# Kernel tuning notes

Hardware: AMD Instinct MI355X
Metric: run time of the kernel (lower is better)

Reference implementation:

```python
import jax, jax.numpy as jnp
import numpy as np
import math

K = 8       # wavelet order (k)
C = 8       # channels (c)
ALPHA = 64  # retained Fourier modes
L = 0       # coarsest level
B = 32
N = 8192    # power of two


def setup_inputs() -> dict:
    key = jax.random.key(0)
    ks = jax.random.split(key, 14)
    ck = C * K
    scale = 1.0 / (ck * ck)  # matches torch: 1/(c*k)**2
    f32 = jnp.float32
    inp = {
        "x": jax.random.normal(ks[0], (B, N, C, K), dtype=f32),
        # SparseKernelFT1d weights (complex, stored as re/im): scale * rand
        "wA_re": scale * jax.random.uniform(ks[1], (ck, ck, ALPHA), dtype=f32),
        "wA_im": scale * jax.random.uniform(ks[2], (ck, ck, ALPHA), dtype=f32),
        "wB_re": scale * jax.random.uniform(ks[3], (ck, ck, ALPHA), dtype=f32),
        "wB_im": scale * jax.random.uniform(ks[4], (ck, ck, ALPHA), dtype=f32),
        "wC_re": scale * jax.random.uniform(ks[5], (ck, ck, ALPHA), dtype=f32),
        "wC_im": scale * jax.random.uniform(ks[6], (ck, ck, ALPHA), dtype=f32),
        # T0 linear layer (k -> k)
        "T0_w": jax.random.normal(ks[7], (K, K), dtype=f32) / math.sqrt(K),
        "T0_b": 0.01 * jax.random.normal(ks[8], (K,), dtype=f32),
        # Legendre wavelet filter buffers: ec_* are [H0.T;H1.T] / [G0.T;G1.T] (2k,k),
        # rc_* are [H0;G0] / [H1;G1] (2k,k). Stand-ins: random orthonormal-ish matrices
        # scaled like wavelet filters (same math regardless of exact values).
        "ec_s": jax.random.normal(ks[9], (2 * K, K), dtype=f32) / math.sqrt(2 * K),
        "ec_d": jax.random.normal(ks[10], (2 * K, K), dtype=f32) / math.sqrt(2 * K),
        "rc_e": jax.random.normal(ks[11], (2 * K, K), dtype=f32) / math.sqrt(2 * K),
        "rc_o": jax.random.normal(ks[12], (2 * K, K), dtype=f32) / math.sqrt(2 * K),
    }
    return inp


def _sparse_ft(x, w_re, w_im):
    # x: [B, N, c, k] -> spectral mixing over first ALPHA rfft modes
    Bb, Nn, c, k = x.shape
    xv = x.reshape(Bb, Nn, c * k).transpose(0, 2, 1)   # [B, ck, N]
    xf = jnp.fft.rfft(xv)                               # [B, ck, N//2+1] complex
    l = min(ALPHA, Nn // 2 + 1)
    W = (w_re[:, :, :l] + 1j * w_im[:, :, :l]).astype(jnp.complex64)
    of = jnp.einsum('bix,iox->box', xf[:, :, :l], W)
    out_ft = jnp.zeros((Bb, c * k, Nn // 2 + 1), dtype=jnp.complex64).at[:, :, :l].set(of)
    xo = jnp.fft.irfft(out_ft, n=Nn)                    # [B, ck, N] real
    return xo.transpose(0, 2, 1).reshape(Bb, Nn, c, k)


def reference(x, wA_re, wA_im, wB_re, wB_im, wC_re, wC_im, T0_w, T0_b,
              ec_s, ec_d, rc_e, rc_o):
    Bb, Nn, c, k = x.shape
    ns = int(math.floor(math.log2(Nn)))
    Ud, Us = [], []
    # --- decomposition ---
    for _ in range(ns - L):
        xa = jnp.concatenate([x[:, ::2], x[:, 1::2]], axis=-1)  # [B, N/2, c, 2k]
        d = xa @ ec_d                                           # [B, N/2, c, k]
        s = xa @ ec_s
        Ud.append(_sparse_ft(d, wA_re, wA_im) + _sparse_ft(s, wB_re, wB_im))
        Us.append(_sparse_ft(d, wC_re, wC_im))
        x = s
    # --- coarsest-level linear ---
    x = x @ T0_w.T + T0_b
    # --- reconstruction (u_s is None branch) ---
    for i in range(ns - 1 - L, -1, -1):
        x = x + Us[i]
        xc = jnp.concatenate([x, Ud[i]], axis=-1)               # [B, n, c, 2k]
        x_e = xc @ rc_e
        x_o = xc @ rc_o
        Bc, Nc, cc, _ = xc.shape
        x = jnp.stack([x_e, x_o], axis=2).reshape(Bc, Nc * 2, cc, K)  # interleave even/odd
    return (x,) + tuple(Ud) + tuple(Us)
```

## Files before the change

### kernel.cpp

```cpp
#include <hip/hip_runtime.h>

#define BB 32
#define CKD 64
#define CC 8
#define KK 8
#define FPW 132

__device__ const int D_FCB[14] = {0,32,48,56,60,62,63,64,65,66,67,68,69,70};
__device__ const int D_TB[14] = {0,64,96,112,120,124,126,127,128,129,130,131,132,133};
__device__ const int D_L[13]  = {64,64,64,64,64,64,33,17,9,5,3,2,1};
__device__ const int D_FTOF[13] = {0,524288,786432,917504,983040,1015808,1032192,
                                   1048576,1064960,1081344,1097728,1114112,1130496};
__device__ const int D_XP[65] = {0,13,25,36,46,56,65,74,83,92,100,108,116,124,132,140,
    148,156,163,170,177,184,191,198,205,212,219,226,233,240,247,254,261,268,274,280,
    286,292,298,304,310,316,322,328,334,340,346,352,358,364,370,376,382,388,394,400,
    406,412,418,424,430,436,442,448,454};

typedef __attribute__((ext_vector_type(4))) short s4v;
typedef __attribute__((ext_vector_type(8))) short s8v;
typedef __attribute__((ext_vector_type(4))) float f4v;

static __device__ __forceinline__ float4 ld4(const float* p){ return *(const float4*)p; }
static __device__ __forceinline__ size_t d_udo(int i){ return 33554432ull - (16777216u >> i); }
static __device__ __forceinline__ size_t d_uso(int i){ return 50329600ull - (16777216u >> i); }
static __device__ __forceinline__ size_t d_tof(int i){ return 128ull * (8192u - (8192u >> i)); }

static __device__ __forceinline__ unsigned short b16(float f) {
    unsigned u = __float_as_uint(f);
    u += 0x7FFFu + ((u >> 16) & 1u);
    return (unsigned short)(u >> 16);
}
static __device__ __forceinline__ float fb16(unsigned short h) {
    return __uint_as_float(((unsigned)h) << 16);
}

__global__ __launch_bounds__(256) void gen_tbl2_k(unsigned short* __restrict__ Th,
        unsigned short* __restrict__ Tl, unsigned short* __restrict__ Tfh,
        unsigned short* __restrict__ Tfl) {
    int lvl = blockIdx.y;
    int nh = 4096 >> lvl;
    int idx = blockIdx.x * 256 + threadIdx.x;
    if (blockIdx.z == 0) {
        if (idx >= nh * 128) return;
        int t = idx >> 7, k = idx & 127, x = k >> 1;
        int l = nh / 2 + 1; if (l > 64) l = 64;
        float v = 0.f;
        if (x < l) {
            int r = (x * t) & (nh - 1);
            float th = 6.283185307179586f * ((float)r / (float)nh);
            float s, c; sincosf(th, &s, &c);
            v = (k & 1) ? s : c;
        }
        unsigned short hi = b16(v);
        unsigned short lo = b16(v - fb16(hi));
        size_t off = d_tof(lvl) + idx;
        Th[off] = hi; Tl[off] = lo;
    } else {
        int nhp = nh < 128 ? 128 : nh;
        if (idx >= 128 * nhp) return;
        int j = idx & 7;
        int lane = (idx >> 3) & 63;
        int mt = (idx >> 9) & 7;
        int kb = idx >> 12;
        int row = mt*16 + (lane & 15);
        int t = kb*32 + (lane >> 4)*8 + j;
        int x = row >> 1;
        int l = nh / 2 + 1; if (l > 64) l = 64;
        float v = 0.f;
        if (x < l && t < nh) {
            int r = (x * t) & (nh - 1);
            float th = 6.283185307179586f * ((float)r / (float)nh);
            float s, c; sincosf(th, &s, &c);
            v = (row & 1) ? -s : c;
        }
        unsigned short hi = b16(v);
        unsigned short lo = b16(v - fb16(hi));
        size_t off = (size_t)D_FTOF[lvl] + idx;
        Tfh[off] = hi; Tfl[off] = lo;
    }
}

__global__ __launch_bounds__(256) void wtr_k(const float* __restrict__ wAr,
        const float* __restrict__ wAi, const float* __restrict__ wBr,
        const float* __restrict__ wBi, const float* __restrict__ wCr,
        const float* __restrict__ wCi, float* __restrict__ wt) {
    int x = blockIdx.x, arr = blockIdx.y;
    const float* W;
    switch (arr) {
        case 0: W = wAr; break;
        case 1: W = wAi; break;
        case 2: W = wBr; break;
        case 3: W = wBi; break;
        case 4: W = wCr; break;
        default: W = wCi; break;
    }
    float* o = wt + ((size_t)arr*64 + x)*4096;
    for (int q = threadIdx.x; q < 4096; q += 256)
        o[q] = W[(size_t)q*64 + x];
}

__global__ __launch_bounds__(256) void decomp_k(const float* __restrict__ xin,
        const float* __restrict__ ecd, const float* __restrict__ ecs,
        float* __restrict__ dslot, float* __restrict__ sslot, int nh) {
    int idx = blockIdx.x * 256 + threadIdx.x;
    if (idx >= BB * nh * CC) return;
    int c = idx & 7;
    int t = (idx >> 3) % nh;
    int b = idx / (nh * CC);
    const float* p0 = xin + ((size_t)b * 2 * nh + 2 * t) * CKD + c * KK;
    float xa[16];
    float4 v;
    v = ld4(p0);      xa[0]=v.x; xa[1]=v.y; xa[2]=v.z; xa[3]=v.w;
    v = ld4(p0+4);    xa[4]=v.x; xa[5]=v.y; xa[6]=v.z; xa[7]=v.w;
    v = ld4(p0+64);   xa[8]=v.x; xa[9]=v.y; xa[10]=v.z; xa[11]=v.w;
    v = ld4(p0+68);   xa[12]=v.x; xa[13]=v.y; xa[14]=v.z; xa[15]=v.w;
    float dd[8], ss[8];
    #pragma unroll
    for (int m = 0; m < 8; m++) { dd[m] = 0.f; ss[m] = 0.f; }
    #pragma unroll
    for (int j = 0; j < 16; j++) {
        float xv = xa[j];
        #pragma unroll
        for (int m = 0; m < 8; m++) {
            dd[m] = fmaf(xv, ecd[j*8+m], dd[m]);
            ss[m] = fmaf(xv, ecs[j*8+m], ss[m]);
        }
    }
    size_t ob = ((size_t)b * nh + t) * CKD + c * KK;
    *(float4*)(dslot+ob)   = make_float4(dd[0],dd[1],dd[2],dd[3]);
    *(float4*)(dslot+ob+4) = make_float4(dd[4],dd[5],dd[6],dd[7]);
    *(float4*)(sslot+ob)   = make_float4(ss[0],ss[1],ss[2],ss[3]);
    *(float4*)(sslot+ob+4) = make_float4(ss[4],ss[5],ss[6],ss[7]);
}

__global__ __launch_bounds__(256) void decomp_small_k(const float* __restrict__ s4base,
        const float* __restrict__ ecd, const float* __restrict__ ecs,
        const float* __restrict__ T0w, const float* __restrict__ T0b,
        float* __restrict__ outbuf, float* __restrict__ xt0) {
    __shared__ float sA[128*64];
    __shared__ float sB[64*64];
    int b = blockIdx.x, tid = threadIdx.x;
    for (int lvl = 5; lvl <= 12; lvl++) {
        int nh = 4096 >> lvl;
        const float* src = (lvl == 5) ? (s4base + (size_t)b*256*CKD)
                                      : (((lvl - 6) & 1) ? sB : sA);
        float* dst = ((lvl - 5) & 1) ? sB : sA;
        float* dG = outbuf + d_udo(lvl) + (size_t)b*nh*CKD;
        float* sG = outbuf + d_uso(lvl) + (size_t)b*nh*CKD;
        for (int q = tid; q < nh*8; q += 256) {
            int c = q & 7, t = q >> 3;
            const float* p0 = src + (size_t)(2*t)*CKD + c*KK;
            float xa[16];
            float4 v;
            v = ld4(p0);      xa[0]=v.x; xa[1]=v.y; xa[2]=v.z; xa[3]=v.w;
            v = ld4(p0+4);    xa[4]=v.x; xa[5]=v.y; xa[6]=v.z; xa[7]=v.w;
            v = ld4(p0+64);   xa[8]=v.x; xa[9]=v.y; xa[10]=v.z; xa[11]=v.w;
            v = ld4(p0+68);   xa[12]=v.x; xa[13]=v.y; xa[14]=v.z; xa[15]=v.w;
            float dd[8], ss[8];
            #pragma unroll
            for (int m = 0; m < 8; m++) { dd[m] = 0.f; ss[m] = 0.f; }
            #pragma unroll
            for (int j = 0; j < 16; j++) {
                float xv = xa[j];
                #pragma unroll
                for (int m = 0; m < 8; m++) {
                    dd[m] = fmaf(xv, ecd[j*8+m], dd[m]);
                    ss[m] = fmaf(xv, ecs[j*8+m], ss[m]);
                }
            }
            size_t ob = (size_t)t * CKD + c * KK;
            *(float4*)(dG+ob)   = make_float4(dd[0],dd[1],dd[2],dd[3]);
            *(float4*)(dG+ob+4) = make_float4(dd[4],dd[5],dd[6],dd[7]);
            *(float4*)(sG+ob)   = make_float4(ss[0],ss[1],ss[2],ss[3]);
            *(float4*)(sG+ob+4) = make_float4(ss[4],ss[5],ss[6],ss[7]);
            float* dl = dst + t*CKD + c*KK;
            #pragma unroll
            for (int j = 0; j < 8; j++) dl[j] = ss[j];
        }
        __syncthreads();
    }
    if (tid < 64) {
        int m = tid & 7, c = tid >> 3;
        const float* xr = sB + c*KK;
        float a = T0b[m];
        #pragma unroll
        for (int j = 0; j < 8; j++) a = fmaf(xr[j], T0w[m*8+j], a);
        xt0[(size_t)b*64 + tid] = a;
    }
}

__global__ __launch_bounds__(256) void fft_fwd_mfma_k(const float* __restrict__ outbuf,
        const unsigned short* __restrict__ Tfh, const unsigned short* __restrict__ Tfl,
        float* __restrict__ xfpf, float2* __restrict__ xf_all) {
    __shared__ unsigned vp[128*FPW];
    int slot = blockIdx.x;
    int lvl = 0;
    while (lvl < 12 && slot >= D_FCB[lvl+1]) lvl++;
    int nh = 4096 >> lvl;
    int ch = D_FCB[lvl+1] - D_FCB[lvl];
    int t0s = (slot - D_FCB[lvl]) * 128;
    int b = blockIdx.y;
    const float* V0 = outbuf + d_udo(lvl) + (size_t)b * nh * CKD;
    const float* V1 = outbuf + d_uso(lvl) + (size_t)b * nh * CKD;
    const unsigned short* THb = Tfh + D_FTOF[lvl];
    const unsigned short* TLb = Tfl + D_FTOF[lvl];
    int tid = threadIdx.x;
    int w = tid >> 6, lane = tid & 63;
    int col = lane & 15, khi = lane >> 4;
    int mt0 = w * 2;
    #pragma unroll
    for (int q = 0; q < 16; q++) {
        int fi = tid + 256*q;
        int tl_ = fi >> 5;
        int t = t0s + tl_;
        int iq = fi & 31;
        int z = iq >> 4;
        int i4 = (iq & 15) * 4;
        const float* Vz = z ? V1 : V0;
        float4 v = make_float4(0.f,0.f,0.f,0.f);
        if (t < nh) v = ld4(Vz + (size_t)t*CKD + i4);
        const float* pv = &v.x;
        int rowb = z*64 + i4;
        #pragma unroll
        for (int j = 0; j < 4; j++) {
            int row = rowb + j;
            float f = pv[j];
            unsigned u = __float_as_uint(f);
            unsigned hi = u & 0xFFFF0000u;
            float r = f - __uint_as_float(hi);
            unsigned lo = __float_as_uint(r) & 0xFFFF0000u;
            int cw = tl_ ^ (((row >> 3) & 7) << 2);
            vp[row*FPW + cw] = (hi >> 16) | lo;
        }
    }
    __syncthreads();
    int rrow[8], rswz[8];
    #pragma unroll
    for (int n = 0; n < 8; n++) {
        rrow[n] = n*16 + col;
        rswz[n] = ((rrow[n] >> 3) & 7) << 2;
    }
    f4v acc[2][8];
    #pragma unroll
    for (int m = 0; m < 2; m++)
        #pragma unroll
        for (int n = 0; n < 8; n++) acc[m][n] = (f4v){0.f,0.f,0.f,0.f};
    int kb0 = (slot - D_FCB[lvl]) * 4;
    #pragma unroll
    for (int kk = 0; kk < 4; kk++) {
        int kb = kb0 + kk;
        s8v ah[2], al[2];
        #pragma unroll
        for (int m = 0; m < 2; m++) {
            size_t fo = (((size_t)kb*8 + (mt0 + m))*64 + lane)*8;
            ah[m] = *(const s8v*)(THb + fo);
            al[m] = *(const s8v*)(TLb + fo);
        }
        int cb = kk*32 + khi*8;
        #pragma unroll
        for (int n = 0; n < 8; n++) {
            const unsigned* pr = vp + rrow[n]*FPW;
            uint4 w0 = *(const uint4*)(pr + (cb ^ rswz[n]));
            uint4 w1 = *(const uint4*)(pr + ((cb + 4) ^ rswz[n]));
            s8v bh, bl;
            const unsigned* pw = &w0.x;
            #pragma unroll
            for (int j = 0; j < 4; j++) {
                bh[j] = (short)(pw[j] & 0xFFFFu);
                bl[j] = (short)(pw[j] >> 16);
            }
            pw = &w1.x;
            #pragma unroll
            for (int j = 0; j < 4; j++) {
                bh[4+j] = (short)(pw[j] & 0xFFFFu);
                bl[4+j] = (short)(pw[j] >> 16);
            }
            #pragma unroll
            for (int m = 0; m < 2; m++) {
                acc[m][n] = __builtin_amdgcn_mfma_f32_16x16x32_bf16(ah[m], bh, acc[m][n], 0,0,0);
                acc[m][n] = __builtin_amdgcn_mfma_f32_16x16x32_bf16(ah[m], bl, acc[m][n], 0,0,0);
                acc[m][n] = __builtin_amdgcn_mfma_f32_16x16x32_bf16(al[m], bh, acc[m][n], 0,0,0);
            }
        }
    }
    if (ch == 1) {
        float* XB = (float*)xf_all + (size_t)lvl*524288 + (size_t)b*16384;
        #pragma unroll
        for (int m = 0; m < 2; m++) {
            int m0 = (mt0 + m)*16 + khi*4;
            #pragma unroll
            for (int n = 0; n < 8; n++) {
                int ic = n*16 + col;
                int z = ic >> 6, i = ic & 63;
                float* X = XB + (size_t)z*8192;
                #pragma unroll
                for (int r = 0; r < 4; r++) {
                    int row = m0 + r;
                    X[(((size_t)(row >> 1)*64 + i) << 1) | (row & 1)] = acc[m][n][r];
                }
            }
        }
    } else {
        #pragma unroll
        for (int m = 0; m < 2; m++) {
            int m0 = (mt0 + m)*16 + khi*4;
            #pragma unroll
            for (int n = 0; n < 8; n++) {
                int ic = n*16 + col;
                int z = ic >> 6, i = ic & 63;
                float* P = xfpf + ((size_t)slot*64 + (size_t)b*2 + z) * 8192;
                #pragma unroll
                for (int r = 0; r < 4; r++)
                    P[(size_t)(m0 + r)*64 + i] = acc[m][n][r];
            }
        }
    }
}

__global__ __launch_bounds__(256) void reduce_fwd_k(const float* __restrict__ xfpf,
        float2* __restrict__ xf_all) {
    int lvl = blockIdx.y;
    int e = blockIdx.x * 256 + threadIdx.x;
    int j = e & 4095;
    int bz = e >> 12;
    int x = j >> 6, i = j & 63;
    int c0 = D_FCB[lvl], c1 = D_FCB[lvl+1];
    float re = 0.f, im = 0.f;
    for (int c = c0; c < c1; c++) {
        size_t base = ((size_t)c*64 + bz) * 8192;
        re += xfpf[base + (size_t)(2*x)*64 + i];
        im += xfpf[base + (size_t)(2*x+1)*64 + i];
    }
    xf_all[(size_t)lvl*262144 + (size_t)bz*4096 + j] = make_float2(re, im);
}

__global__ __launch_bounds__(512) void mix_all_k(const float2* __restrict__ xf_all,
        const float* __restrict__ wt,
        unsigned short* __restrict__ ofh, unsigned short* __restrict__ ofl) {
    int x = 0;
    while (x < 64 && (int)blockIdx.x >= D_XP[x+1]) x++;
    int lvl = blockIdx.x - D_XP[x];
    int nh = 4096 >> lvl;
    const float2* xfL = xf_all + (size_t)lvl*262144;
    int tid = threadIdx.x;
    int o = tid & 63, wq = tid >> 6;
    __shared__ float2 sxd[BB*CKD];
    __shared__ float2 sxs[BB*CKD];
    __shared__ float  swt[6][16*CKD];
    for (int q = tid; q < BB*CKD; q += 512) {
        int b = q >> 6, i = q & 63;
        sxd[q] = xfL[((size_t)b*2 + 0)*4096 + x*64 + i];
        sxs[q] = xfL[((size_t)b*2 + 1)*4096 + x*64 + i];
    }
    float2 aud[4], aus[4];
    #pragma unroll
    for (int j=0;j<4;j++){ aud[j]=make_float2(0.f,0.f); aus[j]=make_float2(0.f,0.f); }
    const float* WTx = wt + (size_t)x*4096;
    for (int ic = 0; ic < 4; ic++) {
        __syncthreads();
        for (int q = tid; q < 6*1024; q += 512) {
            int arr = q >> 10, r = q & 1023;
            swt[arr][r] = WTx[(size_t)arr*262144 + ic*1024 + r];
        }
        __syncthreads();
        #pragma unroll 4
        for (int ii = 0; ii < 16; ii++) {
            float ar = swt[0][ii*64+o], ai_ = swt[1][ii*64+o];
            float br = swt[2][ii*64+o], bi_ = swt[3][ii*64+o];
            float cr = swt[4][ii*64+o], ci_ = swt[5][ii*64+o];
            int i = ic*16 + ii;
            #pragma unroll
            for (int j = 0; j < 4; j++) {
                float2 xd = sxd[(wq*4+j)*64 + i];
                float2 xs = sxs[(wq*4+j)*64 + i];
                aud[j].x += xd.x*ar - xd.y*ai_ + xs.x*br - xs.y*bi_;
                aud[j].y += xd.x*ai_ + xd.y*ar + xs.x*bi_ + xs.y*br;
                aus[j].x += xd.x*cr - xd.y*ci_;
                aus[j].y += xd.x*ci_ + xd.y*cr;
            }
        }
    }
    float w = (x == 0 || 2*x == nh) ? 1.f : 2.f;
    float sc = w / (float)nh;
    int k0 = 2*x;
    #pragma unroll
    for (int j = 0; j < 4; j++) {
        int b = wq*4 + j;
        {
            size_t base = (((size_t)lvl*32 + b)*2 + 0)*8192;
            float A = sc*aud[j].x, Bn = -sc*aud[j].y;
            unsigned short ha = b16(A),  hb = b16(Bn);
            unsigned short la = b16(A - fb16(ha)), lb = b16(Bn - fb16(hb));
            ofh[base + (size_t)k0*64 + o]     = ha;
            ofh[base + (size_t)(k0+1)*64 + o] = hb;
            ofl[base + (size_t)k0*64 + o]     = la;
            ofl[base + (size_t)(k0+1)*64 + o] = lb;
        }
        {
            size_t base = (((size_t)lvl*32 + b)*2 + 1)*8192;
            float A = sc*aus[j].x, Bn = -sc*aus[j].y;
            unsigned short ha = b16(A),  hb = b16(Bn);
            unsigned short la = b16(A - fb16(ha)), lb = b16(Bn - fb16(hb));
            ofh[base + (size_t)k0*64 + o]     = ha;
            ofh[base + (size_t)(k0+1)*64 + o] = hb;
            ofl[base + (size_t)k0*64 + o]     = la;
            ofl[base + (size_t)(k0+1)*64 + o] = lb;
        }
    }
}

__global__ __launch_bounds__(256) void fft_inv_mfma_k(
        const unsigned short* __restrict__ ofh, const unsigned short* __restrict__ ofl,
        const unsigned short* __restrict__ Th,  const unsigned short* __restrict__ Tl,
        float* __restrict__ outbuf) {
    __shared__ unsigned short gh[2*64*132];
    __shared__ unsigned short gl[2*64*132];
    int lvl = 0;
    while (lvl < 12 && (int)blockIdx.x >= D_TB[lvl+1]) lvl++;
    int g = blockIdx.x - D_TB[lvl];
    int nh = 4096 >> lvl;
    int tbase = g * 64;
    int b = blockIdx.y;
    int tid = threadIdx.x;
    #pragma unroll
    for (int q = 0; q < 8; q++) {
        int fi = tid + 256*q;
        int z = fi >> 10;
        int r = fi & 1023;
        int k = r & 127, oct = r >> 7;
        const unsigned short* Gh = ofh + (((size_t)lvl*32 + b)*2 + z)*8192;
        const unsigned short* Gl = ofl + (((size_t)lvl*32 + b)*2 + z)*8192;
        uint4 vh = *(const uint4*)(Gh + (size_t)k*64 + oct*8);
        uint4 vl = *(const uint4*)(Gl + (size_t)k*64 + oct*8);
        const unsigned* ph = &vh.x;
        const unsigned* pl = &vl.x;
        #pragma unroll
        for (int i = 0; i < 8; i++) {
            unsigned wd = ph[i>>1];
            gh[z*8448 + (oct*8+i)*132 + k] = (i&1) ? (unsigned short)(wd>>16) : (unsigned short)(wd&0xFFFF);
            wd = pl[i>>1];
            gl[z*8448 + (oct*8+i)*132 + k] = (i&1) ? (unsigned short)(wd>>16) : (unsigned short)(wd&0xFFFF);
        }
    }
    __syncthreads();
    int w = tid >> 6;
    int lane = tid & 63;
    int tb = tbase + w*16;
    if (tb >= nh) return;
    int trow = lane & 15, khi = lane >> 4;
    int tA = tb + trow; if (tA >= nh) tA = nh - 1;
    const unsigned short* THp = Th + d_tof(lvl) + (size_t)tA*128 + khi*8;
    const unsigned short* TLp = Tl + d_tof(lvl) + (size_t)tA*128 + khi*8;
    f4v acc[8];
    #pragma unroll
    for (int n = 0; n < 8; n++) acc[n] = (f4v){0.f,0.f,0.f,0.f};
    #pragma unroll
    for (int kk = 0; kk < 4; kk++) {
        s8v ah = *(const s8v*)(THp + kk*32);
        s8v al = *(const s8v*)(TLp + kk*32);
        #pragma unroll
        for (int n = 0; n < 8; n++) {
            int z = n >> 2;
            int off = z*8448 + ((n & 3)*16 + trow)*132 + kk*32 + khi*8;
            s4v b0 = *(const s4v*)(gh + off);
            s4v b1 = *(const s4v*)(gh + off + 4);
            s4v c0 = *(const s4v*)(gl + off);
            s4v c1 = *(const s4v*)(gl + off + 4);
            s8v bh = __builtin_shufflevector(b0, b1, 0,1,2,3,4,5,6,7);
            s8v bl = __builtin_shufflevector(c0, c1, 0,1,2,3,4,5,6,7);
            acc[n] = __builtin_amdgcn_mfma_f32_16x16x32_bf16(ah, bh, acc[n], 0, 0, 0);
            acc[n] = __builtin_amdgcn_mfma_f32_16x16x32_bf16(ah, bl, acc[n], 0, 0, 0);
            acc[n] = __builtin_amdgcn_mfma_f32_16x16x32_bf16(al, bh, acc[n], 0, 0, 0);
        }
    }
    float* U0 = outbuf + d_udo(lvl) + (size_t)b * nh * CKD;
    float* U1 = outbuf + d_uso(lvl) + (size_t)b * nh * CKD;
    int thi4 = khi * 4;
    #pragma unroll
    for (int n = 0; n < 8; n++) {
        float* U = (n >> 2) ? U1 : U0;
        int ocol = (n & 3)*16 + trow;
        #pragma unroll
        for (int r = 0; r < 4; r++) {
            int t = tb + thi4 + r;
            if (t < nh) U[(size_t)t*64 + ocol] = acc[n][r];
        }
    }
}

__global__ __launch_bounds__(256) void recon_small_k(const float* __restrict__ xt0,
        const float* __restrict__ outbuf,
        const float* __restrict__ rce, const float* __restrict__ rco,
        float* __restrict__ rb0) {
    __shared__ float xA[128*64];
    __shared__ float xB[64*64];
    int b = blockIdx.x, tid = threadIdx.x;
    if (tid < 64) xB[tid] = xt0[(size_t)b*64 + tid];
    __syncthreads();
    for (int i = 12; i >= 6; i--) {
        int nh = 4096 >> i;
        const float* cur = ((i == 12) || !(i & 1)) ? xB : xA;
        float* nxt = (i & 1) ? xB : xA;
        const float* Us = outbuf + d_uso(i) + (size_t)b*nh*CKD;
        const float* Ud = outbuf + d_udo(i) + (size_t)b*nh*CKD;
        for (int q = tid; q < nh*8; q += 256) {
            int c = q & 7, t = q >> 3;
            size_t base = (size_t)t*CKD + c*KK;
            float xc[16];
            float4 a0 = ld4(cur+base), a1 = ld4(cur+base+4);
            float4 u0 = ld4(Us+base),  u1 = ld4(Us+base+4);
            float4 d0 = ld4(Ud+base),  d1 = ld4(Ud+base+4);
            xc[0]=a0.x+u0.x; xc[1]=a0.y+u0.y; xc[2]=a0.z+u0.z; xc[3]=a0.w+u0.w;
            xc[4]=a1.x+u1.x; xc[5]=a1.y+u1.y; xc[6]=a1.z+u1.z; xc[7]=a1.w+u1.w;
            xc[8]=d0.x;  xc[9]=d0.y;  xc[10]=d0.z; xc[11]=d0.w;
            xc[12]=d1.x; xc[13]=d1.y; xc[14]=d1.z; xc[15]=d1.w;
            float e[8], o2[8];
            #pragma unroll
            for (int m = 0; m < 8; m++) { e[m] = 0.f; o2[m] = 0.f; }
            #pragma unroll
            for (int j = 0; j < 16; j++) {
                float xv = xc[j];
                #pragma unroll
                for (int m = 0; m < 8; m++) {
                    e[m]  = fmaf(xv, rce[j*8+m], e[m]);
                    o2[m] = fmaf(xv, rco[j*8+m], o2[m]);
                }
            }
            if (i > 6) {
                float* pe = nxt + (size_t)(2*t)*CKD + c*KK;
                #pragma unroll
                for (int j = 0; j < 8; j++) { pe[j] = e[j]; pe[CKD + j] = o2[j]; }
            } else {
                float* pe = rb0 + ((size_t)b*128 + 2*t)*CKD + c*KK;
                *(float4*)(pe)      = make_float4(e[0],e[1],e[2],e[3]);
                *(float4*)(pe+4)    = make_float4(e[4],e[5],e[6],e[7]);
                *(float4*)(pe+64)   = make_float4(o2[0],o2[1],o2[2],o2[3]);
                *(float4*)(pe+68)   = make_float4(o2[4],o2[5],o2[6],o2[7]);
            }
        }
        __syncthreads();
    }
}

__global__ __launch_bounds__(256) void recon_k(const float* __restrict__ xin,
        const float* __restrict__ us, const float* __restrict__ ud,
        const float* __restrict__ rce, const float* __restrict__ rco,
        float* __restrict__ xout, int nh) {
    int idx = blockIdx.x*256 + threadIdx.x;
    if (idx >= BB*nh*CC) return;
    int c = idx & 7;
    int t = (idx >> 3) % nh;
    int b = idx / (nh*CC);
    size_t base = ((size_t)b*nh + t)*CKD + c*KK;
    float xc[16];
    float4 a0 = ld4(xin+base), a1 = ld4(xin+base+4);
    float4 u0 = ld4(us+base),  u1 = ld4(us+base+4);
    float4 d0 = ld4(ud+base),  d1 = ld4(ud+base+4);
    xc[0]=a0.x+u0.x; xc[1]=a0.y+u0.y; xc[2]=a0.z+u0.z; xc[3]=a0.w+u0.w;
    xc[4]=a1.x+u1.x; xc[5]=a1.y+u1.y; xc[6]=a1.z+u1.z; xc[7]=a1.w+u1.w;
    xc[8]=d0.x;  xc[9]=d0.y;  xc[10]=d0.z; xc[11]=d0.w;
    xc[12]=d1.x; xc[13]=d1.y; xc[14]=d1.z; xc[15]=d1.w;
    float e[8], o2[8];
    #pragma unroll
    for (int m = 0; m < 8; m++) { e[m] = 0.f; o2[m] = 0.f; }
    #pragma unroll
    for (int j = 0; j < 16; j++) {
        float xv = xc[j];
        #pragma unroll
        for (int m = 0; m < 8; m++) {
            e[m]  = fmaf(xv, rce[j*8+m], e[m]);
            o2[m] = fmaf(xv, rco[j*8+m], o2[m]);
        }
    }
    size_t ob = ((size_t)b*2*nh + 2*t)*CKD + c*KK;
    *(float4*)(xout+ob)      = make_float4(e[0],e[1],e[2],e[3]);
    *(float4*)(xout+ob+4)    = make_float4(e[4],e[5],e[6],e[7]);
    *(float4*)(xout+ob+64)   = make_float4(o2[0],o2[1],o2[2],o2[3]);
    *(float4*)(xout+ob+68)   = make_float4(o2[4],o2[5],o2[6],o2[7]);
}

extern "C" void kernel_launch(void* const* d_in, const int* in_sizes, int n_in,
                              void* d_out, int out_size, void* d_ws, size_t ws_size,
                              hipStream_t stream) {
    const float* x   = (const float*)d_in[0];
    const float* wAr = (const float*)d_in[1];
    const float* wAi = (const float*)d_in[2];
    const float* wBr = (const float*)d_in[3];
    const float* wBi = (const float*)d_in[4];
    const float* wCr = (const float*)d_in[5];
    const float* wCi = (const float*)d_in[6];
    const float* T0w = (const float*)d_in[7];
    const float* T0b = (const float*)d_in[8];
    const float* ecs = (const float*)d_in[9];
    const float* ecd = (const float*)d_in[10];
    const float* rce = (const float*)d_in[11];
    const float* rco = (const float*)d_in[12];
    float* out = (float*)d_out;
    float* wsf = (float*)d_ws;

    size_t p = 0;
    float2* xf_all = (float2*)(wsf + p); p += 6815744;
    unsigned short* ofh = (unsigned short*)(wsf + p); p += 3407872;
    unsigned short* ofl = (unsigned short*)(wsf + p); p += 3407872;
    unsigned short* Th  = (unsigned short*)(wsf + p); p += 528384;
    unsigned short* Tl  = (unsigned short*)(wsf + p); p += 528384;
    unsigned short* Tfh = (unsigned short*)(wsf + p); p += 573440;
    unsigned short* Tfl = (unsigned short*)(wsf + p); p += 573440;
    float*  wt   = wsf + p; p += 1572864;
    float*  xt0  = wsf + p; p += 2048;
    float*  rb0  = wsf + p; p += 4194304;
    float*  rb1  = wsf + p; p += 8388608;
    float*  xfpf = wsf + p; p += 36700160;
    (void)ws_size; (void)in_sizes; (void)n_in; (void)out_size;

    size_t udo[13], uso[13];
    for (int i = 0; i < 13; i++) {
        udo[i] = 33554432ull - (16777216u >> i);
        uso[i] = 50329600ull - (16777216u >> i);
    }

    gen_tbl2_k<<<dim3(2048, 13, 2), 256, 0, stream>>>(Th, Tl, Tfh, Tfl);
    wtr_k<<<dim3(64, 6), 256, 0, stream>>>(wAr, wAi, wBr, wBi, wCr, wCi, wt);

    for (int i = 0; i < 5; i++) {
        int nh = 4096 >> i;
        const float* xin_l = (i == 0) ? x : (out + uso[i-1]);
        int tot = BB * nh * CC;
        decomp_k<<<(tot + 255)/256, 256, 0, stream>>>(xin_l, ecd, ecs, out + udo[i], out + uso[i], nh);
    }
    decomp_small_k<<<BB, 256, 0, stream>>>(out + uso[4], ecd, ecs, T0w, T0b, out, xt0);

    fft_fwd_mfma_k<<<dim3(70, BB), 256, 0, stream>>>(out, Tfh, Tfl, xfpf, xf_all);
    reduce_fwd_k<<<dim3(1024, 5), 256, 0, stream>>>(xfpf, xf_all);
    mix_all_k<<<454, 512, 0, stream>>>(xf_all, wt, ofh, ofl);
    fft_inv_mfma_k<<<dim3(133, BB), 256, 0, stream>>>(ofh, ofl, Th, Tl, out);

    recon_small_k<<<BB, 256, 0, stream>>>(xt0, out, rce, rco, rb0);
    const float* rin = rb0;
    for (int i = 5; i >= 0; i--) {
        int nh = 4096 >> i;
        float* ro = (i == 0) ? out : ((i & 1) ? rb1 : rb0);
        int tot = BB * nh * CC;
        recon_k<<<(tot + 255)/256, 256, 0, stream>>>(rin, out + uso[i], out + udo[i], rce, rco, ro, nh);
        rin = ro;
    }
}
```

Baseline: 477.1 us.

## Run spectral mixing as split-bf16 MFMA GEMM with prepacked real-block weights

Replaces the scalar FP32 complex spectral-mixing kernel with an MFMA kernel. The complex products for the A, B and C weights become one 256x256 real block matrix. That matrix is prepacked per mode into hi/lo bf16 fragments by a new wbig_k kernel. Activations are split into hi/lo bf16 in swizzled shared memory, and three MFMAs per tile approximate FP32 accuracy. This is meant to remove the FP32 FMA bottleneck of the mixing stage, at the cost of an extra packing kernel, about 16 MB more weight traffic, and some zero blocks in the GEMM.

```diff
diff --git a/kernel.cpp b/kernel.cpp
--- a/kernel.cpp
+++ b/kernel.cpp
@@ -97,6 +97,45 @@
     float* o = wt + ((size_t)arr*64 + x)*4096;
     for (int q = threadIdx.x; q < 4096; q += 256)
         o[q] = W[(size_t)q*64 + x];
+}
+
+__global__ __launch_bounds__(256) void wbig_k(const float* __restrict__ wt,
+        unsigned short* __restrict__ wbh, unsigned short* __restrict__ wbl) {
+    int x = blockIdx.x;
+    int f0 = blockIdx.y * 2048;
+    for (int q = threadIdx.x; q < 2048; q += 256) {
+        int f = f0 + q;
+        int j = f & 7;
+        int lane = (f >> 3) & 63;
+        int nt = (f >> 9) & 15;
+        int kt = f >> 13;
+        int k = kt*32 + (lane >> 4)*8 + j;
+        int n = nt*16 + (lane & 15);
+        int pk = k >> 6, i = k & 63;
+        int pn = n >> 6, o = n & 63;
+        int arr; float sgn;
+        switch ((pn << 2) | pk) {
+            case 0:  arr = 0; sgn =  1.f; break;
+            case 1:  arr = 1; sgn = -1.f; break;
+            case 2:  arr = 2; sgn =  1.f; break;
+            case 3:  arr = 3; sgn = -1.f; break;
+            case 4:  arr = 1; sgn = -1.f; break;
+            case 5:  arr = 0; sgn = -1.f; break;
+            case 6:  arr = 3; sgn = -1.f; break;
+            case 7:  arr = 2; sgn = -1.f; break;
+            case 8:  arr = 4; sgn =  1.f; break;
+            case 9:  arr = 5; sgn = -1.f; break;
+            case 12: arr = 5; sgn = -1.f; break;
+            case 13: arr = 4; sgn = -1.f; break;
+            default: arr = -1; sgn = 0.f; break;
+        }
+        float v = 0.f;
+        if (arr >= 0) v = sgn * wt[((size_t)arr*64 + x)*4096 + (size_t)i*64 + o];
+        unsigned short h = b16(v);
+        unsigned short l2 = b16(v - fb16(h));
+        wbh[(size_t)x*65536 + f] = h;
+        wbl[(size_t)x*65536 + f] = l2;
+    }
 }
 
 __global__ __launch_bounds__(256) void decomp_k(const float* __restrict__ xin,
@@ -334,77 +373,92 @@
     xf_all[(size_t)lvl*262144 + (size_t)bz*4096 + j] = make_float2(re, im);
 }
 
-__global__ __launch_bounds__(512) void mix_all_k(const float2* __restrict__ xf_all,
-        const float* __restrict__ wt,
+__global__ __launch_bounds__(256) void mix_mfma_k(const float2* __restrict__ xf_all,
+        const unsigned short* __restrict__ wbh, const unsigned short* __restrict__ wbl,
         unsigned short* __restrict__ ofh, unsigned short* __restrict__ ofl) {
+    __shared__ unsigned ax[32*260];
     int x = 0;
     while (x < 64 && (int)blockIdx.x >= D_XP[x+1]) x++;
     int lvl = blockIdx.x - D_XP[x];
     int nh = 4096 >> lvl;
     const float2* xfL = xf_all + (size_t)lvl*262144;
     int tid = threadIdx.x;
-    int o = tid & 63, wq = tid >> 6;
-    __shared__ float2 sxd[BB*CKD];
-    __shared__ float2 sxs[BB*CKD];
-    __shared__ float  swt[6][16*CKD];
-    for (int q = tid; q < BB*CKD; q += 512) {
-        int b = q >> 6, i = q & 63;
-        sxd[q] = xfL[((size_t)b*2 + 0)*4096 + x*64 + i];
-        sxs[q] = xfL[((size_t)b*2 + 1)*4096 + x*64 + i];
-    }
-    float2 aud[4], aus[4];
-    #pragma unroll
-    for (int j=0;j<4;j++){ aud[j]=make_float2(0.f,0.f); aus[j]=make_float2(0.f,0.f); }
-    const float* WTx = wt + (size_t)x*4096;
-    for (int ic = 0; ic < 4; ic++) {
-        __syncthreads();
-        for (int q = tid; q < 6*1024; q += 512) {
-            int arr = q >> 10, r = q & 1023;
-            swt[arr][r] = WTx[(size_t)arr*262144 + ic*1024 + r];
-        }
-        __syncthreads();
-        #pragma unroll 4
-        for (int ii = 0; ii < 16; ii++) {
-            float ar = swt[0][ii*64+o], ai_ = swt[1][ii*64+o];
-            float br = swt[2][ii*64+o], bi_ = swt[3][ii*64+o];
-            float cr = swt[4][ii*64+o], ci_ = swt[5][ii*64+o];
-            int i = ic*16 + ii;
-            #pragma unroll
-            for (int j = 0; j < 4; j++) {
-                float2 xd = sxd[(wq*4+j)*64 + i];
-                float2 xs = sxs[(wq*4+j)*64 + i];
-                aud[j].x += xd.x*ar - xd.y*ai_ + xs.x*br - xs.y*bi_;
-                aud[j].y += xd.x*ai_ + xd.y*ar + xs.x*bi_ + xs.y*br;
-                aus[j].x += xd.x*cr - xd.y*ci_;
-                aus[j].y += xd.x*ci_ + xd.y*cr;
-            }
-        }
-    }
-    float w = (x == 0 || 2*x == nh) ? 1.f : 2.f;
-    float sc = w / (float)nh;
+    for (int q = tid; q < 4096; q += 256) {
+        int b = q >> 7, z = (q >> 6) & 1, i = q & 63;
+        float2 v = xfL[((size_t)b*2 + z)*4096 + (size_t)x*64 + i];
+        int sw = ((b >> 3) & 7) << 2;
+        int kR = z*128 + i;
+        unsigned uR = __float_as_uint(v.x);
+        unsigned hiR = uR & 0xFFFF0000u;
+        float rR = v.x - __uint_as_float(hiR);
+        unsigned loR = __float_as_uint(rR) & 0xFFFF0000u;
+        ax[b*260 + (kR ^ sw)] = (hiR >> 16) | loR;
+        unsigned uI = __float_as_uint(v.y);
+        unsigned hiI = uI & 0xFFFF0000u;
+        float rI = v.y - __uint_as_float(hiI);
+        unsigned loI = __float_as_uint(rI) & 0xFFFF0000u;
+        ax[b*260 + ((kR + 64) ^ sw)] = (hiI >> 16) | loI;
+    }
+    __syncthreads();
+    int w4 = tid >> 6, lane = tid & 63;
+    int col = lane & 15, khi = lane >> 4;
+    int mt = w4 & 1, nt0 = (w4 >> 1) * 8;
+    int arow = mt*16 + col;
+    int asw = ((arow >> 3) & 7) << 2;
+    const unsigned* ap = ax + arow*260;
+    const unsigned short* WBH = wbh + (size_t)x*65536;
+    const unsigned short* WBL = wbl + (size_t)x*65536;
+    f4v acc[8];
+    #pragma unroll
+    for (int n = 0; n < 8; n++) acc[n] = (f4v){0.f,0.f,0.f,0.f};
+    #pragma unroll
+    for (int kt = 0; kt < 8; kt++) {
+        int cb = kt*32 + khi*8;
+        uint4 a0 = *(const uint4*)(ap + (cb ^ asw));
+        uint4 a1 = *(const uint4*)(ap + ((cb + 4) ^ asw));
+        s8v ah, al;
+        const unsigned* pw = &a0.x;
+        #pragma unroll
+        for (int j = 0; j < 4; j++) {
+            ah[j] = (short)(pw[j] & 0xFFFFu);
+            al[j] = (short)(pw[j] >> 16);
+        }
+        pw = &a1.x;
+        #pragma unroll
+        for (int j = 0; j < 4; j++) {
+            ah[4+j] = (short)(pw[j] & 0xFFFFu);
+            al[4+j] = (short)(pw[j] >> 16);
+        }
+        #pragma unroll
+        for (int n = 0; n < 8; n++) {
+            int nt = nt0 + n;
+            size_t fo = (((size_t)kt*16 + nt)*64 + lane)*8;
+            s8v bh = *(const s8v*)(WBH + fo);
+            s8v bl = *(const s8v*)(WBL + fo);
+            acc[n] = __builtin_amdgcn_mfma_f32_16x16x32_bf16(ah, bh, acc[n], 0, 0, 0);
+            acc[n] = __builtin_amdgcn_mfma_f32_16x16x32_bf16(ah, bl, acc[n], 0, 0, 0);
+            acc[n] = __builtin_amdgcn_mfma_f32_16x16x32_bf16(al, bh, acc[n], 0, 0, 0);
+        }
+    }
+    float wfac = (x == 0 || 2*x == nh) ? 1.f : 2.f;
+    float sc = wfac / (float)nh;
     int k0 = 2*x;
     #pragma unroll
-    for (int j = 0; j < 4; j++) {
-        int b = wq*4 + j;
-        {
-            size_t base = (((size_t)lvl*32 + b)*2 + 0)*8192;
-            float A = sc*aud[j].x, Bn = -sc*aud[j].y;
-            unsigned short ha = b16(A),  hb = b16(Bn);
-            unsigned short la = b16(A - fb16(ha)), lb = b16(Bn - fb16(hb));
-            ofh[base + (size_t)k0*64 + o]     = ha;
-            ofh[base + (size_t)(k0+1)*64 + o] = hb;
-            ofl[base + (size_t)k0*64 + o]     = la;
-            ofl[base + (size_t)(k0+1)*64 + o] = lb;
-        }
-        {
-            size_t base = (((size_t)lvl*32 + b)*2 + 1)*8192;
-            float A = sc*aus[j].x, Bn = -sc*aus[j].y;
-            unsigned short ha = b16(A),  hb = b16(Bn);
-            unsigned short la = b16(A - fb16(ha)), lb = b16(Bn - fb16(hb));
-            ofh[base + (size_t)k0*64 + o]     = ha;
-            ofh[base + (size_t)(k0+1)*64 + o] = hb;
-            ofl[base + (size_t)k0*64 + o]     = la;
-            ofl[base + (size_t)(k0+1)*64 + o] = lb;
+    for (int n = 0; n < 8; n++) {
+        int nn = nt0 + n;
+        int pn = nn >> 2;
+        int o = (nn & 3)*16 + col;
+        int z = pn >> 1;
+        int kr = k0 + (pn & 1);
+        #pragma unroll
+        for (int r = 0; r < 4; r++) {
+            int b = mt*16 + khi*4 + r;
+            size_t base = (((size_t)lvl*32 + b)*2 + z)*8192 + (size_t)kr*64 + o;
+            float v = sc * acc[n][r];
+            unsigned short h = b16(v);
+            unsigned short l2 = b16(v - fb16(h));
+            ofh[base] = h;
+            ofl[base] = l2;
         }
     }
 }
@@ -607,6 +661,8 @@
     unsigned short* Tfh = (unsigned short*)(wsf + p); p += 573440;
     unsigned short* Tfl = (unsigned short*)(wsf + p); p += 573440;
     float*  wt   = wsf + p; p += 1572864;
+    unsigned short* wbh = (unsigned short*)(wsf + p); p += 2097152;
+    unsigned short* wbl = (unsigned short*)(wsf + p); p += 2097152;
     float*  xt0  = wsf + p; p += 2048;
     float*  rb0  = wsf + p; p += 4194304;
     float*  rb1  = wsf + p; p += 8388608;
@@ -621,6 +677,7 @@
 
     gen_tbl2_k<<<dim3(2048, 13, 2), 256, 0, stream>>>(Th, Tl, Tfh, Tfl);
     wtr_k<<<dim3(64, 6), 256, 0, stream>>>(wAr, wAi, wBr, wBi, wCr, wCi, wt);
+    wbig_k<<<dim3(64, 32), 256, 0, stream>>>(wt, wbh, wbl);
 
     for (int i = 0; i < 5; i++) {
         int nh = 4096 >> i;
@@ -632,7 +689,7 @@
 
     fft_fwd_mfma_k<<<dim3(70, BB), 256, 0, stream>>>(out, Tfh, Tfl, xfpf, xf_all);
     reduce_fwd_k<<<dim3(1024, 5), 256, 0, stream>>>(xfpf, xf_all);
-    mix_all_k<<<454, 512, 0, stream>>>(xf_all, wt, ofh, ofl);
+    mix_mfma_k<<<454, 256, 0, stream>>>(xf_all, wbh, wbl, ofh, ofl);
     fft_inv_mfma_k<<<dim3(133, BB), 256, 0, stream>>>(ofh, ofl, Th, Tl, out);
 
     recon_small_k<<<BB, 256, 0, stream>>>(xt0, out, rce, rco, rb0);
```

Result: faster. 434.4 us (-9.0%).
